# Kernel optimization log

Hardware: AMD Instinct MI355X
Metric: run time of the kernel (lower is better)

The kernel has to match this reference:

```python
import jax, jax.numpy as jnp
import numpy as np

EPS = 1e-5  # torch LayerNorm default


def setup_inputs() -> dict:
    key = jax.random.key(0)
    k1, k2, k3 = jax.random.split(key, 3)
    B, C, O, M, H, Wd = 4, 64, 64, 4, 384, 384
    x = jax.random.normal(k1, (B, C, H, Wd), dtype=jnp.float32)
    # DNM_W is [M, out, in, 1, 1] -> flattened 1x1 conv weights [M, out, in]
    W = jax.random.uniform(k2, (M, O, C), dtype=jnp.float32)
    q = jax.random.uniform(k3, (1,), dtype=jnp.float32)
    gamma = jnp.ones((C,), jnp.float32)   # LayerNorm weight (norm1)
    beta = jnp.zeros((C,), jnp.float32)   # LayerNorm bias (norm1)
    return {"x": x, "W": W, "q": q, "gamma": gamma, "beta": beta}


def reference(x, W, q, gamma, beta):
    # x: [B, C, H, W]; LayerNorm over channel dim (module permutes to NHWC first)
    xt = jnp.transpose(x, (0, 2, 3, 1))            # [B, H, W, C]
    mu = jnp.mean(xt, axis=-1, keepdims=True)
    var = jnp.var(xt, axis=-1, keepdims=True)      # biased, matches torch
    xn = (xt - mu) * jax.lax.rsqrt(var + EPS) * gamma + beta
    # M parallel 1x1 convs == per-pixel matmuls, batched into one einsum
    y = jnp.einsum('bhwc,moc->mbhwo', xn, W)       # [M, B, H, W, O]
    out = jnp.sum(jnp.maximum(y - q, 0.0), axis=0) # relu(conv - q), sum over M
    return jnp.transpose(out, (0, 3, 1, 2))        # [B, O, H, W]
```

## Files before the change

### kernel.cpp

```cpp
#include <hip/hip_runtime.h>
#include <hip/hip_bf16.h>

typedef __attribute__((ext_vector_type(8))) short short8;
typedef __attribute__((ext_vector_type(4))) float f32x4;
typedef __attribute__((ext_vector_type(4))) unsigned int u32x4;

#define HWPIX 147456
#define NC 64
#define NO 64
#define NM 4
#define EPSV 1e-5f

static __device__ __forceinline__ unsigned int cvt_pk(float a, float b) {
    unsigned int r;
    asm("v_cvt_pk_bf16_f32 %0, %1, %2" : "=v"(r) : "v"(a), "v"(b));
    return r;
}

#define BAR() do { asm volatile("s_waitcnt lgkmcnt(0)" ::: "memory"); \
                   __builtin_amdgcn_s_barrier();                      \
                   asm volatile("" ::: "memory"); } while (0)

__global__ __launch_bounds__(256) void dnm_fused(
    const float* __restrict__ x, const float* __restrict__ Wg,
    const float* __restrict__ qp, const float* __restrict__ gamma,
    const float* __restrict__ beta, float* __restrict__ out)
{
    __shared__ __align__(16) unsigned char lds[2][8192];

    const int tid = threadIdx.x;
    const int wv  = tid >> 6;
    const int ln  = tid & 63;
    const int p16 = ln & 15;
    const int g4  = ln >> 4;

    const int bid = blockIdx.x;
    const int b       = bid / 288;
    const int pixbase = (bid % 288) * 512;

    const float qv = qp[0];
    const float q4 = 4.0f * qv;

    f32x4 gA[2], gB[2], bA[2], bB[2];
#pragma unroll
    for (int ch = 0; ch < 2; ++ch) {
        gA[ch] = *(const f32x4*)(gamma + ch * 32 + g4 * 8);
        gB[ch] = *(const f32x4*)(gamma + ch * 32 + g4 * 8 + 4);
        bA[ch] = *(const f32x4*)(beta  + ch * 32 + g4 * 8);
        bB[ch] = *(const f32x4*)(beta  + ch * 32 + g4 * 8 + 4);
    }
    short8 wh[NM][2];
    float bias[NM];
#pragma unroll
    for (int m = 0; m < NM; ++m) {
        float bsum = 0.f;
#pragma unroll
        for (int ch = 0; ch < 2; ++ch) {
            const float* wp = Wg + ((m * NO + (wv * 16 + p16)) * NC + ch * 32 + g4 * 8);
            f32x4 a = *(const f32x4*)(wp);
            f32x4 c = *(const f32x4*)(wp + 4);
            float f[8]  = {a[0], a[1], a[2], a[3], c[0], c[1], c[2], c[3]};
            float gg[8] = {gA[ch][0], gA[ch][1], gA[ch][2], gA[ch][3],
                           gB[ch][0], gB[ch][1], gB[ch][2], gB[ch][3]};
            float bb[8] = {bA[ch][0], bA[ch][1], bA[ch][2], bA[ch][3],
                           bB[ch][0], bB[ch][1], bB[ch][2], bB[ch][3]};
            float wq[8];
#pragma unroll
            for (int j = 0; j < 8; ++j) {
                bsum += bb[j] * f[j];
                wq[j] = gg[j] * f[j];
            }
            u32x4 hu;
#pragma unroll
            for (int p = 0; p < 4; ++p) hu[p] = cvt_pk(wq[2*p], wq[2*p+1]);
            wh[m][ch] = __builtin_bit_cast(short8, hu);
        }
        bsum += __shfl_xor(bsum, 16);
        bsum += __shfl_xor(bsum, 32);
        bias[m] = bsum;
    }

    const float* xpl = x + (size_t)b * NC * HWPIX + pixbase + wv * 16 + p16
                         + (size_t)(g4 * 16) * HWPIX;
    float* const outw = out + (size_t)b * NO * HWPIX
                            + (size_t)(wv * 16 + p16) * HWPIX + pixbase;

    const int r  = wv * 16 + p16;
    const int rk = r & 7;

    float xv[16];
#pragma unroll
    for (int i = 0; i < 16; ++i) xv[i] = xpl[(size_t)i * HWPIX];

#pragma unroll 1
    for (int it = 0; it < 8; ++it) {
        unsigned char* buf = lds[it & 1];

        {
            float s1 = 0.f, s2 = 0.f;
#pragma unroll
            for (int i = 0; i < 16; ++i) { s1 += xv[i]; s2 += xv[i] * xv[i]; }
            s1 += __shfl_xor(s1, 16);  s2 += __shfl_xor(s2, 16);
            s1 += __shfl_xor(s1, 32);  s2 += __shfl_xor(s2, 32);
            const float mu  = s1 * (1.f / 64.f);
            const float var = s2 * (1.f / 64.f) - mu * mu;
            const float rs  = rsqrtf(var + EPSV);
            u32x4 h0, h1;
#pragma unroll
            for (int p = 0; p < 4; ++p) {
                h0[p] = cvt_pk((xv[2*p]     - mu) * rs, (xv[2*p+1] - mu) * rs);
                h1[p] = cvt_pk((xv[8+2*p]   - mu) * rs, (xv[9+2*p] - mu) * rs);
            }
            const int s0 = g4 * 2;
            *(u32x4*)(buf + r * 128 + (((s0    ) ^ rk) << 4)) = h0;
            *(u32x4*)(buf + r * 128 + (((s0 + 1) ^ rk) << 4)) = h1;
        }
        BAR();

        if (it < 7) {
            const float* xp = xpl + (it + 1) * 64;
#pragma unroll
            for (int i = 0; i < 16; ++i) xv[i] = xp[(size_t)i * HWPIX];
        }

#pragma unroll 1
        for (int ps = 0; ps < 4; ++ps) {
            const int row = ps * 16 + p16;
            const int rwk = row & 7;
            short8 ah[2];
#pragma unroll
            for (int ch = 0; ch < 2; ++ch) {
                const int slot = ch * 4 + g4;
                ah[ch] = *(const short8*)(buf + row * 128 + ((slot ^ rwk) << 4));
            }
            f32x4 acc[NM];
#pragma unroll
            for (int m = 0; m < NM; ++m) {
                f32x4 a = {bias[m], bias[m], bias[m], bias[m]};
#pragma unroll
                for (int ch = 0; ch < 2; ++ch) {
                    a = __builtin_amdgcn_mfma_f32_16x16x32_bf16(ah[ch], wh[m][ch], a, 0, 0, 0);
                }
                acc[m] = a;
            }
            f32x4 v;
#pragma unroll
            for (int rr = 0; rr < 4; ++rr) {
                v[rr] = (fmaxf(acc[0][rr], qv) + fmaxf(acc[1][rr], qv))
                      + (fmaxf(acc[2][rr], qv) + fmaxf(acc[3][rr], qv)) - q4;
            }
            __builtin_nontemporal_store(
                v, (f32x4*)(outw + it * 64 + ps * 16 + g4 * 4));
        }
    }
}

extern "C" void kernel_launch(void* const* d_in, const int* in_sizes, int n_in,
                              void* d_out, int out_size, void* d_ws, size_t ws_size,
                              hipStream_t stream) {
    const float* x     = (const float*)d_in[0];
    const float* Wg    = (const float*)d_in[1];
    const float* q     = (const float*)d_in[2];
    const float* gamma = (const float*)d_in[3];
    const float* beta  = (const float*)d_in[4];
    float* out = (float*)d_out;

    dnm_fused<<<dim3(1152), dim3(256), 0, stream>>>(x, Wg, q, gamma, beta, out);
}
```

Before: 70.24 us.

## Remove LDS staging by giving each wave its own pixels and all output channels

Each wave now owns its own 128-pixel slice and computes all 64 output channels. It keeps all 32 bf16 weight fragments in registers and feeds the normalized activations straight into MFMA as the A operand. The channel-to-lane mapping is chosen so that the normalized registers line up with the MFMA K layout. This removes the LDS transpose writes and reads and the block barrier each iteration. In exchange it uses many more registers for weights, which may reduce occupancy. Global stores also become narrower, 16 pixels per row per iteration instead of 64.

```diff
diff --git a/kernel.cpp b/kernel.cpp
--- a/kernel.cpp
+++ b/kernel.cpp
@@ -17,17 +17,11 @@
     return r;
 }
 
-#define BAR() do { asm volatile("s_waitcnt lgkmcnt(0)" ::: "memory"); \
-                   __builtin_amdgcn_s_barrier();                      \
-                   asm volatile("" ::: "memory"); } while (0)
-
 __global__ __launch_bounds__(256) void dnm_fused(
     const float* __restrict__ x, const float* __restrict__ Wg,
     const float* __restrict__ qp, const float* __restrict__ gamma,
     const float* __restrict__ beta, float* __restrict__ out)
 {
-    __shared__ __align__(16) unsigned char lds[2][8192];
-
     const int tid = threadIdx.x;
     const int wv  = tid >> 6;
     const int ln  = tid & 63;
@@ -36,7 +30,7 @@
 
     const int bid = blockIdx.x;
     const int b       = bid / 288;
-    const int pixbase = (bid % 288) * 512;
+    const int pixbase = (bid % 288) * 512 + wv * 128;
 
     const float qv = qp[0];
     const float q4 = 4.0f * qv;
@@ -49,97 +43,89 @@
         bA[ch] = *(const f32x4*)(beta  + ch * 32 + g4 * 8);
         bB[ch] = *(const f32x4*)(beta  + ch * 32 + g4 * 8 + 4);
     }
-    short8 wh[NM][2];
-    float bias[NM];
+    short8 wh[NM][4][2];
+    float  bias[NM][4];
 #pragma unroll
     for (int m = 0; m < NM; ++m) {
-        float bsum = 0.f;
 #pragma unroll
-        for (int ch = 0; ch < 2; ++ch) {
-            const float* wp = Wg + ((m * NO + (wv * 16 + p16)) * NC + ch * 32 + g4 * 8);
-            f32x4 a = *(const f32x4*)(wp);
-            f32x4 c = *(const f32x4*)(wp + 4);
-            float f[8]  = {a[0], a[1], a[2], a[3], c[0], c[1], c[2], c[3]};
-            float gg[8] = {gA[ch][0], gA[ch][1], gA[ch][2], gA[ch][3],
-                           gB[ch][0], gB[ch][1], gB[ch][2], gB[ch][3]};
-            float bb[8] = {bA[ch][0], bA[ch][1], bA[ch][2], bA[ch][3],
-                           bB[ch][0], bB[ch][1], bB[ch][2], bB[ch][3]};
-            float wq[8];
+        for (int os = 0; os < 4; ++os) {
+            float bsum = 0.f;
 #pragma unroll
-            for (int j = 0; j < 8; ++j) {
-                bsum += bb[j] * f[j];
-                wq[j] = gg[j] * f[j];
+            for (int ch = 0; ch < 2; ++ch) {
+                const float* wp = Wg + ((m * NO + (os * 16 + p16)) * NC + ch * 32 + g4 * 8);
+                f32x4 a = *(const f32x4*)(wp);
+                f32x4 c = *(const f32x4*)(wp + 4);
+                float f[8]  = {a[0], a[1], a[2], a[3], c[0], c[1], c[2], c[3]};
+                float gg[8] = {gA[ch][0], gA[ch][1], gA[ch][2], gA[ch][3],
+                               gB[ch][0], gB[ch][1], gB[ch][2], gB[ch][3]};
+                float bb[8] = {bA[ch][0], bA[ch][1], bA[ch][2], bA[ch][3],
+                               bB[ch][0], bB[ch][1], bB[ch][2], bB[ch][3]};
+                float wq[8];
+#pragma unroll
+                for (int j = 0; j < 8; ++j) {
+                    bsum += bb[j] * f[j];
+                    wq[j] = gg[j] * f[j];
+                }
+                u32x4 hu;
+#pragma unroll
+                for (int p = 0; p < 4; ++p) hu[p] = cvt_pk(wq[2*p], wq[2*p+1]);
+                wh[m][os][ch] = __builtin_bit_cast(short8, hu);
             }
-            u32x4 hu;
-#pragma unroll
-            for (int p = 0; p < 4; ++p) hu[p] = cvt_pk(wq[2*p], wq[2*p+1]);
-            wh[m][ch] = __builtin_bit_cast(short8, hu);
+            bsum += __shfl_xor(bsum, 16);
+            bsum += __shfl_xor(bsum, 32);
+            bias[m][os] = bsum;
         }
-        bsum += __shfl_xor(bsum, 16);
-        bsum += __shfl_xor(bsum, 32);
-        bias[m] = bsum;
     }
 
-    const float* xpl = x + (size_t)b * NC * HWPIX + pixbase + wv * 16 + p16
-                         + (size_t)(g4 * 16) * HWPIX;
-    float* const outw = out + (size_t)b * NO * HWPIX
-                            + (size_t)(wv * 16 + p16) * HWPIX + pixbase;
-
-    const int r  = wv * 16 + p16;
-    const int rk = r & 7;
+    const float* xpl = x + (size_t)b * NC * HWPIX + pixbase + p16
+                         + (size_t)(g4 * 8) * HWPIX;
+    float* const outw = out + (size_t)b * NO * HWPIX + (size_t)p16 * HWPIX
+                            + pixbase + g4 * 4;
 
     float xv[16];
 #pragma unroll
-    for (int i = 0; i < 16; ++i) xv[i] = xpl[(size_t)i * HWPIX];
+    for (int j = 0; j < 8; ++j) {
+        xv[j]     = xpl[(size_t)j * HWPIX];
+        xv[8 + j] = xpl[(size_t)(32 + j) * HWPIX];
+    }
 
 #pragma unroll 1
     for (int it = 0; it < 8; ++it) {
-        unsigned char* buf = lds[it & 1];
+        float s1 = 0.f, s2 = 0.f;
+#pragma unroll
+        for (int i = 0; i < 16; ++i) { s1 += xv[i]; s2 += xv[i] * xv[i]; }
+        s1 += __shfl_xor(s1, 16);  s2 += __shfl_xor(s2, 16);
+        s1 += __shfl_xor(s1, 32);  s2 += __shfl_xor(s2, 32);
+        const float mu  = s1 * (1.f / 64.f);
+        const float var = s2 * (1.f / 64.f) - mu * mu;
+        const float rs  = rsqrtf(var + EPSV);
 
-        {
-            float s1 = 0.f, s2 = 0.f;
+        u32x4 h0, h1;
 #pragma unroll
-            for (int i = 0; i < 16; ++i) { s1 += xv[i]; s2 += xv[i] * xv[i]; }
-            s1 += __shfl_xor(s1, 16);  s2 += __shfl_xor(s2, 16);
-            s1 += __shfl_xor(s1, 32);  s2 += __shfl_xor(s2, 32);
-            const float mu  = s1 * (1.f / 64.f);
-            const float var = s2 * (1.f / 64.f) - mu * mu;
-            const float rs  = rsqrtf(var + EPSV);
-            u32x4 h0, h1;
-#pragma unroll
-            for (int p = 0; p < 4; ++p) {
-                h0[p] = cvt_pk((xv[2*p]     - mu) * rs, (xv[2*p+1] - mu) * rs);
-                h1[p] = cvt_pk((xv[8+2*p]   - mu) * rs, (xv[9+2*p] - mu) * rs);
-            }
-            const int s0 = g4 * 2;
-            *(u32x4*)(buf + r * 128 + (((s0    ) ^ rk) << 4)) = h0;
-            *(u32x4*)(buf + r * 128 + (((s0 + 1) ^ rk) << 4)) = h1;
+        for (int p = 0; p < 4; ++p) {
+            h0[p] = cvt_pk((xv[2*p]   - mu) * rs, (xv[2*p+1] - mu) * rs);
+            h1[p] = cvt_pk((xv[8+2*p] - mu) * rs, (xv[9+2*p] - mu) * rs);
         }
-        BAR();
+        short8 ah[2] = {__builtin_bit_cast(short8, h0), __builtin_bit_cast(short8, h1)};
 
         if (it < 7) {
-            const float* xp = xpl + (it + 1) * 64;
+            const float* xp = xpl + (it + 1) * 16;
 #pragma unroll
-            for (int i = 0; i < 16; ++i) xv[i] = xp[(size_t)i * HWPIX];
+            for (int j = 0; j < 8; ++j) {
+                xv[j]     = xp[(size_t)j * HWPIX];
+                xv[8 + j] = xp[(size_t)(32 + j) * HWPIX];
+            }
         }
 
-#pragma unroll 1
-        for (int ps = 0; ps < 4; ++ps) {
-            const int row = ps * 16 + p16;
-            const int rwk = row & 7;
-            short8 ah[2];
 #pragma unroll
-            for (int ch = 0; ch < 2; ++ch) {
-                const int slot = ch * 4 + g4;
-                ah[ch] = *(const short8*)(buf + row * 128 + ((slot ^ rwk) << 4));
-            }
+        for (int os = 0; os < 4; ++os) {
             f32x4 acc[NM];
 #pragma unroll
             for (int m = 0; m < NM; ++m) {
-                f32x4 a = {bias[m], bias[m], bias[m], bias[m]};
+                f32x4 a = {bias[m][os], bias[m][os], bias[m][os], bias[m][os]};
 #pragma unroll
                 for (int ch = 0; ch < 2; ++ch) {
-                    a = __builtin_amdgcn_mfma_f32_16x16x32_bf16(ah[ch], wh[m][ch], a, 0, 0, 0);
+                    a = __builtin_amdgcn_mfma_f32_16x16x32_bf16(ah[ch], wh[m][os][ch], a, 0, 0, 0);
                 }
                 acc[m] = a;
             }
@@ -150,7 +136,7 @@
                       + (fmaxf(acc[2][rr], qv) + fmaxf(acc[3][rr], qv)) - q4;
             }
             __builtin_nontemporal_store(
-                v, (f32x4*)(outw + it * 64 + ps * 16 + g4 * 4));
+                v, (f32x4*)(outw + (size_t)(os * 16) * HWPIX + it * 16));
         }
     }
 }
```

Measured after the change: 111.8 us. 1.59x slower.

## Stage x tiles into LDS with async global_load_lds double buffering

Applied to the files above, without the earlier changes.

Replaces per-thread strided 4-byte register loads of the input with 16-byte global_load_lds transfers into a double-buffered, XOR-swizzled LDS staging area. The next tile is issued before the current tile is processed, with vmcnt waits and barriers ordering the stages. Threads then read their channel values back from LDS for the LayerNorm. The normalized bf16 fragment buffer becomes single-buffered. The aim is wider, better-coalesced loads and more memory-level parallelism without holding prefetched values in registers. The cost is extra LDS traffic, more LDS footprint and an additional barrier per iteration.

```diff
diff --git a/kernel.cpp b/kernel.cpp
--- a/kernel.cpp
+++ b/kernel.cpp
@@ -17,16 +17,19 @@
     return r;
 }
 
-#define BAR() do { asm volatile("s_waitcnt lgkmcnt(0)" ::: "memory"); \
-                   __builtin_amdgcn_s_barrier();                      \
-                   asm volatile("" ::: "memory"); } while (0)
+static __device__ __forceinline__ void gll16(const float* g, unsigned char* l) {
+    __builtin_amdgcn_global_load_lds(
+        (const __attribute__((address_space(1))) unsigned int*)g,
+        (__attribute__((address_space(3))) unsigned int*)l, 16, 0, 0);
+}
 
 __global__ __launch_bounds__(256) void dnm_fused(
     const float* __restrict__ x, const float* __restrict__ Wg,
     const float* __restrict__ qp, const float* __restrict__ gamma,
     const float* __restrict__ beta, float* __restrict__ out)
 {
-    __shared__ __align__(16) unsigned char lds[2][8192];
+    __shared__ __align__(16) unsigned char xraw[2][16384];
+    __shared__ __align__(16) unsigned char frag[8192];
 
     const int tid = threadIdx.x;
     const int wv  = tid >> 6;
@@ -80,23 +83,48 @@
         bias[m] = bsum;
     }
 
-    const float* xpl = x + (size_t)b * NC * HWPIX + pixbase + wv * 16 + p16
-                         + (size_t)(g4 * 16) * HWPIX;
+    const int kw   = (5 * wv) & 15;
+    const int cl   = ln >> 4;
+    const int qsrc = (ln & 15) ^ kw;
+    const float* gsrc[4];
+#pragma unroll
+    for (int i = 0; i < 4; ++i)
+        gsrc[i] = x + (size_t)b * NC * HWPIX
+                    + (size_t)(wv * 16 + i * 4 + cl) * HWPIX
+                    + pixbase + qsrc * 4;
+
     float* const outw = out + (size_t)b * NO * HWPIX
                             + (size_t)(wv * 16 + p16) * HWPIX + pixbase;
 
     const int r  = wv * 16 + p16;
     const int rk = r & 7;
 
-    float xv[16];
+    auto STAGE = [&](int t, int bsel) {
 #pragma unroll
-    for (int i = 0; i < 16; ++i) xv[i] = xpl[(size_t)i * HWPIX];
+        for (int i = 0; i < 4; ++i)
+            gll16(gsrc[i] + t * 64, &xraw[bsel][(wv * 16 + i * 4) * 256]);
+    };
+
+    STAGE(0, 0);
 
 #pragma unroll 1
-    for (int it = 0; it < 8; ++it) {
-        unsigned char* buf = lds[it & 1];
+    for (int t = 0; t < 8; ++t) {
+        const unsigned char* braw = xraw[t & 1];
+        if (t < 7) STAGE(t + 1, (t + 1) & 1);
+
+        if (t == 0 || t == 7) asm volatile("s_waitcnt vmcnt(4)" ::: "memory");
+        else                  asm volatile("s_waitcnt vmcnt(8)" ::: "memory");
+        __builtin_amdgcn_s_barrier();
+        asm volatile("" ::: "memory");
 
         {
+            const int s = ((wv * 4 + (p16 >> 2)) ^ ((5 * g4) & 15));
+            const unsigned char* rbase = braw + (g4 * 16) * 256 + s * 16 + (p16 & 3) * 4;
+            float xv[16];
+#pragma unroll
+            for (int ic = 0; ic < 16; ++ic)
+                xv[ic] = *(const float*)(rbase + ic * 256);
+
             float s1 = 0.f, s2 = 0.f;
 #pragma unroll
             for (int i = 0; i < 16; ++i) { s1 += xv[i]; s2 += xv[i] * xv[i]; }
@@ -112,16 +140,12 @@
                 h1[p] = cvt_pk((xv[8+2*p]   - mu) * rs, (xv[9+2*p] - mu) * rs);
             }
             const int s0 = g4 * 2;
-            *(u32x4*)(buf + r * 128 + (((s0    ) ^ rk) << 4)) = h0;
-            *(u32x4*)(buf + r * 128 + (((s0 + 1) ^ rk) << 4)) = h1;
+            *(u32x4*)(frag + r * 128 + (((s0    ) ^ rk) << 4)) = h0;
+            *(u32x4*)(frag + r * 128 + (((s0 + 1) ^ rk) << 4)) = h1;
         }
-        BAR();
-
-        if (it < 7) {
-            const float* xp = xpl + (it + 1) * 64;
-#pragma unroll
-            for (int i = 0; i < 16; ++i) xv[i] = xp[(size_t)i * HWPIX];
-        }
+        asm volatile("s_waitcnt lgkmcnt(0)" ::: "memory");
+        __builtin_amdgcn_s_barrier();
+        asm volatile("" ::: "memory");
 
 #pragma unroll 1
         for (int ps = 0; ps < 4; ++ps) {
@@ -131,7 +155,7 @@
 #pragma unroll
             for (int ch = 0; ch < 2; ++ch) {
                 const int slot = ch * 4 + g4;
-                ah[ch] = *(const short8*)(buf + row * 128 + ((slot ^ rwk) << 4));
+                ah[ch] = *(const short8*)(frag + row * 128 + ((slot ^ rwk) << 4));
             }
             f32x4 acc[NM];
 #pragma unroll
@@ -150,8 +174,9 @@
                       + (fmaxf(acc[2][rr], qv) + fmaxf(acc[3][rr], qv)) - q4;
             }
             __builtin_nontemporal_store(
-                v, (f32x4*)(outw + it * 64 + ps * 16 + g4 * 4));
+                v, (f32x4*)(outw + t * 64 + ps * 16 + g4 * 4));
         }
+        asm volatile("" ::: "memory");
     }
 }
 
```

Result: no change. 69.48 us (median of 2 runs) (-1.1%).
